# Kernel optimization log

Measured on AMD Instinct MI355X. Metric: run time of the kernel, lower is better.

Reference implementation:

```python
import jax, jax.numpy as jnp
import numpy as np

B, S, D = 32, 2048, 1024

def setup_inputs() -> dict:
    key = jax.random.key(0)
    k1, k2, k3 = jax.random.split(key, 3)
    embed_output = jax.random.normal(k1, (B, S, D), dtype=jnp.float32)
    mask = jax.random.randint(k2, (B, S), 0, 2) > 0  # bool [B,S]
    w = jax.random.normal(k3, (D, D), dtype=jnp.float32) * 0.05
    return {"embed_output": embed_output, "mask": mask, "w": w}

def reference(embed_output, mask, w):
    # ys: mean over sequence (NOTE: original does NOT mask the mean) -> [B,1,D]
    ys = jnp.mean(embed_output, axis=-2, keepdims=True)
    maskf = mask.astype(jnp.float32)
    # eW = (E @ W) * mask  -> [B,S,D]
    eW = jnp.einsum('bsd,de->bse', embed_output, w) * maskf[..., None]
    # f = dot(eW, ys) over last axis -> [B,S,1]
    f = jnp.sum(eW * ys, axis=-1, keepdims=True)
    # additive -1e9 bias where mask is False
    f = f + ((1.0 - maskf) * -1.0e9)[..., None]
    # softmax over sequence axis (-2)
    f = jax.nn.softmax(f, axis=-2)
    # weighted sum over sequence -> [B,D]
    zs = jnp.sum(f * embed_output, axis=-2)
    return zs, f
```

## Files before the change

### kernel.cpp

```cpp
#include <hip/hip_runtime.h>
#include <hip/hip_bf16.h>

#define B_ 32
#define S_ 2048
#define D_ 1024
#define NCH 16

__global__ void probe_mask(const unsigned int* __restrict__ m, int* __restrict__ flag) {
    int tid = threadIdx.x;
    bool isI = true, isF = true;
    for (int i = tid * 4; i < tid * 4 + 4; ++i) {
        unsigned v = m[i];
        if (v > 1u) isI = false;
        if (v != 0u && v != 0x3F800000u) isF = false;
    }
    unsigned long long bi = __ballot(isI);
    unsigned long long bf = __ballot(isF);
    if (tid == 0) {
        int f = 0;
        if (bi == ~0ull) f = 1;
        else if (bf == ~0ull) f = 2;
        *flag = f;
    }
}

__global__ __launch_bounds__(256) void k1_colsum(const float* __restrict__ E,
                                                 float* __restrict__ part_sums) {
    int chunk = blockIdx.x, b = blockIdx.y, tid = threadIdx.x;
    const float4* base =
        (const float4*)(E + (size_t)(b * S_ + chunk * (S_ / NCH)) * D_);
    float4 acc = make_float4(0.f, 0.f, 0.f, 0.f);
    for (int i = 0; i < S_ / NCH; ++i) {
        float4 e = base[(size_t)i * (D_ / 4) + tid];
        acc.x += e.x; acc.y += e.y; acc.z += e.z; acc.w += e.w;
    }
    ((float4*)part_sums)[(size_t)(b * NCH + chunk) * (D_ / 4) + tid] = acc;
}

__global__ void k2a_ys(const float* __restrict__ part_sums, float* __restrict__ ys) {
    int g = blockIdx.x * 256 + threadIdx.x;
    int b = g >> 10, d = g & (D_ - 1);
    float s = 0.f;
    for (int k = 0; k < NCH; ++k) s += part_sums[(size_t)(b * NCH + k) * D_ + d];
    ys[g] = s * (1.0f / S_);
}

__global__ __launch_bounds__(256) void k2b_v(const float* __restrict__ w,
                                             const float* __restrict__ ys,
                                             float* __restrict__ v) {
    int b = blockIdx.y;
    int d = blockIdx.x * 256 + threadIdx.x;
    const float4* wrow = (const float4*)(w + (size_t)d * D_);
    const float4* yb = (const float4*)(ys + (size_t)b * D_);
    float acc = 0.f;
#pragma unroll 4
    for (int e = 0; e < D_ / 4; ++e) {
        float4 wv = wrow[e], yv = yb[e];
        acc += wv.x * yv.x + wv.y * yv.y + wv.z * yv.z + wv.w * yv.w;
    }
    v[(size_t)b * D_ + d] = acc;
}

__global__ __launch_bounds__(256) void k3_fused(
    const float* __restrict__ E, const void* __restrict__ maskp,
    const float* __restrict__ v, const int* __restrict__ flagp,
    float* __restrict__ logits, float* __restrict__ part_m,
    float* __restrict__ part_l, float* __restrict__ part_z) {
    int chunk = blockIdx.x, b = blockIdx.y;
    int tid = threadIdx.x, wave = tid >> 6, lane = tid & 63;
    int mf = *flagp;
    const int* mi = (const int*)maskp;
    const unsigned char* mu = (const unsigned char*)maskp;
    const float* mfl = (const float*)maskp;

    const float4* vf = (const float4*)(v + (size_t)b * D_);
    float4 v0 = vf[lane], v1 = vf[64 + lane], v2 = vf[128 + lane], v3 = vf[192 + lane];

    float m = -3.0e38f, l = 0.0f;
    float4 z0 = make_float4(0.f, 0.f, 0.f, 0.f), z1 = z0, z2 = z0, z3 = z0;

    int sbase = chunk * (S_ / NCH) + wave * 32;
    for (int i = 0; i < 32; ++i) {
        int s = sbase + i;
        const float4* row = (const float4*)(E + (size_t)(b * S_ + s) * D_);
        float4 e0 = row[lane], e1 = row[64 + lane], e2 = row[128 + lane], e3 = row[192 + lane];
        float p = e0.x * v0.x + e0.y * v0.y + e0.z * v0.z + e0.w * v0.w;
        p += e1.x * v1.x + e1.y * v1.y + e1.z * v1.z + e1.w * v1.w;
        p += e2.x * v2.x + e2.y * v2.y + e2.z * v2.z + e2.w * v2.w;
        p += e3.x * v3.x + e3.y * v3.y + e3.z * v3.z + e3.w * v3.w;
#pragma unroll
        for (int off = 32; off; off >>= 1) p += __shfl_xor(p, off, 64);
        int idx = b * S_ + s;
        int mv = (mf == 1) ? (mi[idx] != 0)
                           : (mf == 2 ? (mfl[idx] != 0.0f) : (mu[idx] != 0));
        float logit = mv ? p : -1.0e9f;
        if (lane == 0) logits[idx] = logit;
        if (logit > m) {
            float sc = __expf(m - logit);
            l *= sc;
            z0.x *= sc; z0.y *= sc; z0.z *= sc; z0.w *= sc;
            z1.x *= sc; z1.y *= sc; z1.z *= sc; z1.w *= sc;
            z2.x *= sc; z2.y *= sc; z2.z *= sc; z2.w *= sc;
            z3.x *= sc; z3.y *= sc; z3.z *= sc; z3.w *= sc;
            m = logit;
        }
        float pe = __expf(logit - m);
        l += pe;
        z0.x += pe * e0.x; z0.y += pe * e0.y; z0.z += pe * e0.z; z0.w += pe * e0.w;
        z1.x += pe * e1.x; z1.y += pe * e1.y; z1.z += pe * e1.z; z1.w += pe * e1.w;
        z2.x += pe * e2.x; z2.y += pe * e2.y; z2.z += pe * e2.z; z2.w += pe * e2.w;
        z3.x += pe * e3.x; z3.y += pe * e3.y; z3.z += pe * e3.z; z3.w += pe * e3.w;
    }

    __shared__ float lm[4], ll[4];
    __shared__ float4 zbuf[4][256];
    if (lane == 0) { lm[wave] = m; ll[wave] = l; }
    __syncthreads();
    float mb = fmaxf(fmaxf(lm[0], lm[1]), fmaxf(lm[2], lm[3]));
    float lsum = ll[0] * __expf(lm[0] - mb) + ll[1] * __expf(lm[1] - mb) +
                 ll[2] * __expf(lm[2] - mb) + ll[3] * __expf(lm[3] - mb);
    float sc2 = __expf(m - mb);
    zbuf[wave][lane]       = make_float4(z0.x * sc2, z0.y * sc2, z0.z * sc2, z0.w * sc2);
    zbuf[wave][64 + lane]  = make_float4(z1.x * sc2, z1.y * sc2, z1.z * sc2, z1.w * sc2);
    zbuf[wave][128 + lane] = make_float4(z2.x * sc2, z2.y * sc2, z2.z * sc2, z2.w * sc2);
    zbuf[wave][192 + lane] = make_float4(z3.x * sc2, z3.y * sc2, z3.z * sc2, z3.w * sc2);
    __syncthreads();
    float4 a0 = zbuf[0][tid], a1 = zbuf[1][tid], a2 = zbuf[2][tid], a3 = zbuf[3][tid];
    float4 r = make_float4(a0.x + a1.x + a2.x + a3.x, a0.y + a1.y + a2.y + a3.y,
                           a0.z + a1.z + a2.z + a3.z, a0.w + a1.w + a2.w + a3.w);
    ((float4*)(part_z + (size_t)(b * NCH + chunk) * D_))[tid] = r;
    if (tid == 0) { part_m[b * NCH + chunk] = mb; part_l[b * NCH + chunk] = lsum; }
}

__global__ __launch_bounds__(256) void k4_merge(
    const float* __restrict__ part_m, const float* __restrict__ part_l,
    const float* __restrict__ part_z, float* __restrict__ out_zs,
    float* __restrict__ mg, float* __restrict__ lg) {
    int b = blockIdx.x, tid = threadIdx.x;
    float mb = -3.0e38f;
    for (int i = 0; i < NCH; ++i) mb = fmaxf(mb, part_m[b * NCH + i]);
    float lsum = 0.f;
    for (int i = 0; i < NCH; ++i)
        lsum += part_l[b * NCH + i] * __expf(part_m[b * NCH + i] - mb);
    float4 acc = make_float4(0.f, 0.f, 0.f, 0.f);
    for (int i = 0; i < NCH; ++i) {
        float scl = __expf(part_m[b * NCH + i] - mb);
        float4 zv = ((const float4*)(part_z + (size_t)(b * NCH + i) * D_))[tid];
        acc.x += scl * zv.x; acc.y += scl * zv.y;
        acc.z += scl * zv.z; acc.w += scl * zv.w;
    }
    float inv = 1.0f / lsum;
    ((float4*)(out_zs + (size_t)b * D_))[tid] =
        make_float4(acc.x * inv, acc.y * inv, acc.z * inv, acc.w * inv);
    if (tid == 0) { mg[b] = mb; lg[b] = lsum; }
}

__global__ void k5_f(const float* __restrict__ logits, const float* __restrict__ mg,
                     const float* __restrict__ lg, float* __restrict__ out_f) {
    int g = blockIdx.x * 256 + threadIdx.x;
    int b = g >> 11;
    out_f[g] = __expf(logits[g] - mg[b]) * (1.0f / lg[b]);
}

extern "C" void kernel_launch(void* const* d_in, const int* in_sizes, int n_in,
                              void* d_out, int out_size, void* d_ws, size_t ws_size,
                              hipStream_t stream) {
    const float* E = (const float*)d_in[0];
    const void* maskp = d_in[1];
    const float* w = (const float*)d_in[2];
    float* out = (float*)d_out;

    float* ws = (float*)d_ws;
    float* part_sums = ws;
    float* ys = part_sums + (size_t)B_ * NCH * D_;
    float* v = ys + (size_t)B_ * D_;
    float* logits = v + (size_t)B_ * D_;
    float* part_m = logits + (size_t)B_ * S_;
    float* part_l = part_m + B_ * NCH;
    float* part_z = part_l + B_ * NCH;
    float* mg = part_z + (size_t)B_ * NCH * D_;
    float* lg = mg + B_;
    int* flag = (int*)(lg + B_);

    probe_mask<<<1, 64, 0, stream>>>((const unsigned int*)maskp, flag);
    k1_colsum<<<dim3(NCH, B_), 256, 0, stream>>>(E, part_sums);
    k2a_ys<<<(B_ * D_) / 256, 256, 0, stream>>>(part_sums, ys);
    k2b_v<<<dim3(D_ / 256, B_), 256, 0, stream>>>(w, ys, v);
    k3_fused<<<dim3(NCH, B_), 256, 0, stream>>>(E, maskp, v, flag, logits,
                                                part_m, part_l, part_z);
    k4_merge<<<B_, 256, 0, stream>>>(part_m, part_l, part_z, out, mg, lg);
    k5_f<<<(B_ * S_) / 256, 256, 0, stream>>>(logits, mg, lg, out + B_ * D_);
}
```

Baseline: 454.1 us.

## Raise grid parallelism in colsum and fused softmax, coalesce W·ys matvec

The column-sum kernel now splits the sequence into 64 chunks instead of 16, and the fused softmax kernel into 128 chunks of 16 rows. Each block loads its rows up front and computes one block-wide max and weight set, which replaces the per-row online rescaling. The matvec now assigns one wave per W row with coalesced loads, reused across all batches. The aim is more blocks in flight and more memory-level parallelism on the two passes over E. The cost is larger partial buffers and more merge work in k4.

Result: slower. 487.7 us (+7.4%).

```diff
diff --git a/kernel.cpp b/kernel.cpp
--- a/kernel.cpp
+++ b/kernel.cpp
@@ -4,7 +4,8 @@
 #define B_ 32
 #define S_ 2048
 #define D_ 1024
-#define NCH 16
+#define NCH1 64
+#define NCH3 128
 
 __global__ void probe_mask(const unsigned int* __restrict__ m, int* __restrict__ flag) {
     int tid = threadIdx.x;
@@ -28,37 +29,43 @@
                                                  float* __restrict__ part_sums) {
     int chunk = blockIdx.x, b = blockIdx.y, tid = threadIdx.x;
     const float4* base =
-        (const float4*)(E + (size_t)(b * S_ + chunk * (S_ / NCH)) * D_);
+        (const float4*)(E + (size_t)(b * S_ + chunk * (S_ / NCH1)) * D_);
     float4 acc = make_float4(0.f, 0.f, 0.f, 0.f);
-    for (int i = 0; i < S_ / NCH; ++i) {
+#pragma unroll 4
+    for (int i = 0; i < S_ / NCH1; ++i) {
         float4 e = base[(size_t)i * (D_ / 4) + tid];
         acc.x += e.x; acc.y += e.y; acc.z += e.z; acc.w += e.w;
     }
-    ((float4*)part_sums)[(size_t)(b * NCH + chunk) * (D_ / 4) + tid] = acc;
+    ((float4*)part_sums)[(size_t)(b * NCH1 + chunk) * (D_ / 4) + tid] = acc;
 }
 
 __global__ void k2a_ys(const float* __restrict__ part_sums, float* __restrict__ ys) {
     int g = blockIdx.x * 256 + threadIdx.x;
     int b = g >> 10, d = g & (D_ - 1);
     float s = 0.f;
-    for (int k = 0; k < NCH; ++k) s += part_sums[(size_t)(b * NCH + k) * D_ + d];
+#pragma unroll 8
+    for (int k = 0; k < NCH1; ++k) s += part_sums[(size_t)(b * NCH1 + k) * D_ + d];
     ys[g] = s * (1.0f / S_);
 }
 
 __global__ __launch_bounds__(256) void k2b_v(const float* __restrict__ w,
                                              const float* __restrict__ ys,
                                              float* __restrict__ v) {
-    int b = blockIdx.y;
-    int d = blockIdx.x * 256 + threadIdx.x;
+    int tid = threadIdx.x, wave = tid >> 6, lane = tid & 63;
+    int d = blockIdx.x * 4 + wave;
     const float4* wrow = (const float4*)(w + (size_t)d * D_);
-    const float4* yb = (const float4*)(ys + (size_t)b * D_);
-    float acc = 0.f;
-#pragma unroll 4
-    for (int e = 0; e < D_ / 4; ++e) {
-        float4 wv = wrow[e], yv = yb[e];
-        acc += wv.x * yv.x + wv.y * yv.y + wv.z * yv.z + wv.w * yv.w;
-    }
-    v[(size_t)b * D_ + d] = acc;
+    float4 w0 = wrow[lane], w1 = wrow[64 + lane], w2 = wrow[128 + lane], w3 = wrow[192 + lane];
+    for (int b = 0; b < B_; ++b) {
+        const float4* yb = (const float4*)(ys + (size_t)b * D_);
+        float4 y0 = yb[lane], y1 = yb[64 + lane], y2 = yb[128 + lane], y3 = yb[192 + lane];
+        float p = w0.x * y0.x + w0.y * y0.y + w0.z * y0.z + w0.w * y0.w;
+        p += w1.x * y1.x + w1.y * y1.y + w1.z * y1.z + w1.w * y1.w;
+        p += w2.x * y2.x + w2.y * y2.y + w2.z * y2.z + w2.w * y2.w;
+        p += w3.x * y3.x + w3.y * y3.y + w3.z * y3.z + w3.w * y3.w;
+#pragma unroll
+        for (int off = 32; off; off >>= 1) p += __shfl_xor(p, off, 64);
+        if (lane == 0) v[(size_t)b * D_ + d] = p;
+    }
 }
 
 __global__ __launch_bounds__(256) void k3_fused(
@@ -76,60 +83,75 @@
     const float4* vf = (const float4*)(v + (size_t)b * D_);
     float4 v0 = vf[lane], v1 = vf[64 + lane], v2 = vf[128 + lane], v3 = vf[192 + lane];
 
-    float m = -3.0e38f, l = 0.0f;
-    float4 z0 = make_float4(0.f, 0.f, 0.f, 0.f), z1 = z0, z2 = z0, z3 = z0;
-
-    int sbase = chunk * (S_ / NCH) + wave * 32;
-    for (int i = 0; i < 32; ++i) {
-        int s = sbase + i;
-        const float4* row = (const float4*)(E + (size_t)(b * S_ + s) * D_);
-        float4 e0 = row[lane], e1 = row[64 + lane], e2 = row[128 + lane], e3 = row[192 + lane];
-        float p = e0.x * v0.x + e0.y * v0.y + e0.z * v0.z + e0.w * v0.w;
-        p += e1.x * v1.x + e1.y * v1.y + e1.z * v1.z + e1.w * v1.w;
-        p += e2.x * v2.x + e2.y * v2.y + e2.z * v2.z + e2.w * v2.w;
-        p += e3.x * v3.x + e3.y * v3.y + e3.z * v3.z + e3.w * v3.w;
+    int s0 = chunk * 16 + wave * 4;
+    const float4* row0 = (const float4*)(E + (size_t)(b * S_ + s0) * D_);
+
+    float4 e[4][4];
+#pragma unroll
+    for (int i = 0; i < 4; ++i) {
+        const float4* row = row0 + (size_t)i * (D_ / 4);
+        e[i][0] = row[lane]; e[i][1] = row[64 + lane];
+        e[i][2] = row[128 + lane]; e[i][3] = row[192 + lane];
+    }
+    float lg4[4];
+#pragma unroll
+    for (int i = 0; i < 4; ++i) {
+        float p = e[i][0].x * v0.x + e[i][0].y * v0.y + e[i][0].z * v0.z + e[i][0].w * v0.w;
+        p += e[i][1].x * v1.x + e[i][1].y * v1.y + e[i][1].z * v1.z + e[i][1].w * v1.w;
+        p += e[i][2].x * v2.x + e[i][2].y * v2.y + e[i][2].z * v2.z + e[i][2].w * v2.w;
+        p += e[i][3].x * v3.x + e[i][3].y * v3.y + e[i][3].z * v3.z + e[i][3].w * v3.w;
 #pragma unroll
         for (int off = 32; off; off >>= 1) p += __shfl_xor(p, off, 64);
-        int idx = b * S_ + s;
+        int idx = b * S_ + s0 + i;
         int mv = (mf == 1) ? (mi[idx] != 0)
                            : (mf == 2 ? (mfl[idx] != 0.0f) : (mu[idx] != 0));
-        float logit = mv ? p : -1.0e9f;
-        if (lane == 0) logits[idx] = logit;
-        if (logit > m) {
-            float sc = __expf(m - logit);
-            l *= sc;
-            z0.x *= sc; z0.y *= sc; z0.z *= sc; z0.w *= sc;
-            z1.x *= sc; z1.y *= sc; z1.z *= sc; z1.w *= sc;
-            z2.x *= sc; z2.y *= sc; z2.z *= sc; z2.w *= sc;
-            z3.x *= sc; z3.y *= sc; z3.z *= sc; z3.w *= sc;
-            m = logit;
+        lg4[i] = mv ? p : -1.0e9f;
+    }
+
+    __shared__ float4 slog4[4];
+    __shared__ float swgt[16];
+    if (lane == 0) {
+        float4 lf = make_float4(lg4[0], lg4[1], lg4[2], lg4[3]);
+        slog4[wave] = lf;
+        *(float4*)(logits + (size_t)b * S_ + s0) = lf;
+    }
+    __syncthreads();
+
+    if (wave == 0 && lane < 16) {
+        const float* slog = (const float*)slog4;
+        float m = -3.0e38f;
+#pragma unroll
+        for (int i = 0; i < 16; ++i) m = fmaxf(m, slog[i]);
+        float wv = __expf(slog[lane] - m);
+        swgt[lane] = wv;
+        float l = wv;
+#pragma unroll
+        for (int off = 1; off < 16; off <<= 1) l += __shfl_xor(l, off, 64);
+        if (lane == 0) {
+            part_m[b * NCH3 + chunk] = m;
+            part_l[b * NCH3 + chunk] = l;
         }
-        float pe = __expf(logit - m);
-        l += pe;
-        z0.x += pe * e0.x; z0.y += pe * e0.y; z0.z += pe * e0.z; z0.w += pe * e0.w;
-        z1.x += pe * e1.x; z1.y += pe * e1.y; z1.z += pe * e1.z; z1.w += pe * e1.w;
-        z2.x += pe * e2.x; z2.y += pe * e2.y; z2.z += pe * e2.z; z2.w += pe * e2.w;
-        z3.x += pe * e3.x; z3.y += pe * e3.y; z3.z += pe * e3.z; z3.w += pe * e3.w;
-    }
-
-    __shared__ float lm[4], ll[4];
+    }
+    __syncthreads();
+
+    float4 z0 = make_float4(0.f, 0.f, 0.f, 0.f), z1 = z0, z2 = z0, z3 = z0;
+#pragma unroll
+    for (int i = 0; i < 4; ++i) {
+        float pe = swgt[wave * 4 + i];
+        z0.x += pe * e[i][0].x; z0.y += pe * e[i][0].y; z0.z += pe * e[i][0].z; z0.w += pe * e[i][0].w;
+        z1.x += pe * e[i][1].x; z1.y += pe * e[i][1].y; z1.z += pe * e[i][1].z; z1.w += pe * e[i][1].w;
+        z2.x += pe * e[i][2].x; z2.y += pe * e[i][2].y; z2.z += pe * e[i][2].z; z2.w += pe * e[i][2].w;
+        z3.x += pe * e[i][3].x; z3.y += pe * e[i][3].y; z3.z += pe * e[i][3].z; z3.w += pe * e[i][3].w;
+    }
+
     __shared__ float4 zbuf[4][256];
-    if (lane == 0) { lm[wave] = m; ll[wave] = l; }
-    __syncthreads();
-    float mb = fmaxf(fmaxf(lm[0], lm[1]), fmaxf(lm[2], lm[3]));
-    float lsum = ll[0] * __expf(lm[0] - mb) + ll[1] * __expf(lm[1] - mb) +
-                 ll[2] * __expf(lm[2] - mb) + ll[3] * __expf(lm[3] - mb);
-    float sc2 = __expf(m - mb);
-    zbuf[wave][lane]       = make_float4(z0.x * sc2, z0.y * sc2, z0.z * sc2, z0.w * sc2);
-    zbuf[wave][64 + lane]  = make_float4(z1.x * sc2, z1.y * sc2, z1.z * sc2, z1.w * sc2);
-    zbuf[wave][128 + lane] = make_float4(z2.x * sc2, z2.y * sc2, z2.z * sc2, z2.w * sc2);
-    zbuf[wave][192 + lane] = make_float4(z3.x * sc2, z3.y * sc2, z3.z * sc2, z3.w * sc2);
+    zbuf[wave][lane] = z0; zbuf[wave][64 + lane] = z1;
+    zbuf[wave][128 + lane] = z2; zbuf[wave][192 + lane] = z3;
     __syncthreads();
     float4 a0 = zbuf[0][tid], a1 = zbuf[1][tid], a2 = zbuf[2][tid], a3 = zbuf[3][tid];
     float4 r = make_float4(a0.x + a1.x + a2.x + a3.x, a0.y + a1.y + a2.y + a3.y,
                            a0.z + a1.z + a2.z + a3.z, a0.w + a1.w + a2.w + a3.w);
-    ((float4*)(part_z + (size_t)(b * NCH + chunk) * D_))[tid] = r;
-    if (tid == 0) { part_m[b * NCH + chunk] = mb; part_l[b * NCH + chunk] = lsum; }
+    ((float4*)(part_z + (size_t)(b * NCH3 + chunk) * D_))[tid] = r;
 }
 
 __global__ __launch_bounds__(256) void k4_merge(
@@ -137,15 +159,22 @@
     const float* __restrict__ part_z, float* __restrict__ out_zs,
     float* __restrict__ mg, float* __restrict__ lg) {
     int b = blockIdx.x, tid = threadIdx.x;
+    __shared__ float pm_s[NCH3], pl_s[NCH3], scl_s[NCH3];
+    if (tid < NCH3) {
+        pm_s[tid] = part_m[b * NCH3 + tid];
+        pl_s[tid] = part_l[b * NCH3 + tid];
+    }
+    __syncthreads();
     float mb = -3.0e38f;
-    for (int i = 0; i < NCH; ++i) mb = fmaxf(mb, part_m[b * NCH + i]);
+    for (int i = 0; i < NCH3; ++i) mb = fmaxf(mb, pm_s[i]);
+    if (tid < NCH3) scl_s[tid] = __expf(pm_s[tid] - mb);
+    __syncthreads();
     float lsum = 0.f;
-    for (int i = 0; i < NCH; ++i)
-        lsum += part_l[b * NCH + i] * __expf(part_m[b * NCH + i] - mb);
+    for (int i = 0; i < NCH3; ++i) lsum += pl_s[i] * scl_s[i];
     float4 acc = make_float4(0.f, 0.f, 0.f, 0.f);
-    for (int i = 0; i < NCH; ++i) {
-        float scl = __expf(part_m[b * NCH + i] - mb);
-        float4 zv = ((const float4*)(part_z + (size_t)(b * NCH + i) * D_))[tid];
+    for (int i = 0; i < NCH3; ++i) {
+        float scl = scl_s[i];
+        float4 zv = ((const float4*)(part_z + (size_t)(b * NCH3 + i) * D_))[tid];
         acc.x += scl * zv.x; acc.y += scl * zv.y;
         acc.z += scl * zv.z; acc.w += scl * zv.w;
     }
@@ -172,22 +201,22 @@
 
     float* ws = (float*)d_ws;
     float* part_sums = ws;
-    float* ys = part_sums + (size_t)B_ * NCH * D_;
+    float* ys = part_sums + (size_t)B_ * NCH1 * D_;
     float* v = ys + (size_t)B_ * D_;
     float* logits = v + (size_t)B_ * D_;
     float* part_m = logits + (size_t)B_ * S_;
-    float* part_l = part_m + B_ * NCH;
-    float* part_z = part_l + B_ * NCH;
-    float* mg = part_z + (size_t)B_ * NCH * D_;
+    float* part_l = part_m + B_ * NCH3;
+    float* part_z = part_l + B_ * NCH3;
+    float* mg = part_z + (size_t)B_ * NCH3 * D_;
     float* lg = mg + B_;
     int* flag = (int*)(lg + B_);
 
     probe_mask<<<1, 64, 0, stream>>>((const unsigned int*)maskp, flag);
-    k1_colsum<<<dim3(NCH, B_), 256, 0, stream>>>(E, part_sums);
+    k1_colsum<<<dim3(NCH1, B_), 256, 0, stream>>>(E, part_sums);
     k2a_ys<<<(B_ * D_) / 256, 256, 0, stream>>>(part_sums, ys);
-    k2b_v<<<dim3(D_ / 256, B_), 256, 0, stream>>>(w, ys, v);
-    k3_fused<<<dim3(NCH, B_), 256, 0, stream>>>(E, maskp, v, flag, logits,
-                                                part_m, part_l, part_z);
+    k2b_v<<<D_ / 4, 256, 0, stream>>>(w, ys, v);
+    k3_fused<<<dim3(NCH3, B_), 256, 0, stream>>>(E, maskp, v, flag, logits,
+                                                 part_m, part_l, part_z);
     k4_merge<<<B_, 256, 0, stream>>>(part_m, part_l, part_z, out, mg, lg);
     k5_f<<<(B_ * S_) / 256, 256, 0, stream>>>(logits, mg, lg, out + B_ * D_);
 }
```
